# Kernel optimization log

Measured on AMD Instinct MI355X. Metric: run time of the kernel, lower is better.

## Reference

```python
import jax, jax.numpy as jnp
import numpy as np

B, T, S, I, H = 64, 64, 512, 512, 512

def setup_inputs() -> dict:
    key = jax.random.key(0)
    ks = jax.random.split(key, 9)
    sc = 0.02
    return {
        "input": jax.random.normal(ks[0], (B, T, I), jnp.float32),
        "h0": jax.random.normal(ks[1], (B, H), jnp.float32),
        "c0": jax.random.normal(ks[2], (B, H), jnp.float32),
        "ctx": jax.random.normal(ks[3], (S, B, H), jnp.float32),
        "W_ih": jax.random.normal(ks[4], (4 * H, I), jnp.float32) * sc,
        "b_ih": jax.random.normal(ks[5], (4 * H,), jnp.float32) * sc,
        "W_hh": jax.random.normal(ks[6], (4 * H, H), jnp.float32) * sc,
        "b_hh": jax.random.normal(ks[7], (4 * H,), jnp.float32) * sc,
        "W_out": jax.random.normal(ks[8], (H, 2 * H), jnp.float32) * sc,
    }

def reference(input, h0, c0, ctx, W_ih, b_ih, W_hh, b_hh, W_out):
    ctx_b = ctx.transpose(1, 0, 2)          # (B, S, H)
    x_tm = input.transpose(1, 0, 2)          # (T, B, I) time-major

    def step(carry, x):
        hx, cx = carry
        gates = x @ W_ih.T + b_ih + hx @ W_hh.T + b_hh   # (B, 4H)
        i, f, g, o = jnp.split(gates, 4, axis=1)          # chunk order: in, forget, cell, out
        ct = jax.nn.sigmoid(f) * cx + jax.nn.sigmoid(i) * jnp.tanh(g)
        ht = jax.nn.sigmoid(o) * jnp.tanh(ct)
        # dot attention over source positions
        scores = jnp.einsum('bsh,bh->bs', ctx_b, ht)      # (B, S)
        attn = jax.nn.softmax(scores, axis=1)
        wc = jnp.einsum('bs,bsh->bh', attn, ctx_b)        # (B, H)
        h_tilde = jnp.tanh(jnp.concatenate([wc, ht], axis=1) @ W_out.T)
        return (ht, ct), h_tilde

    (hT, cT), out = jax.lax.scan(step, (h0, c0), x_tm)    # out: (T, B, H)
    return out.transpose(1, 0, 2), hT, cT
```

## Files before the change

kernel.cpp:

```cpp
#include <hip/hip_runtime.h>
#include <hip/hip_bf16.h>

#define NB 64
#define NT_ 64
#define NS 512
#define NI 512
#define NH 512
#define G4 2048
#define H2 1024
#define BT (NB*NT_)
#define RBLK 64
#define CPB 8
#define XWB 512
#define TRB 4096
#define WOB 128
#define GRID_MEGA (RBLK + XWB + TRB + WOB)

typedef __attribute__((ext_vector_type(8))) short short8;
typedef __attribute__((ext_vector_type(4))) float f32x4;

__device__ __forceinline__ short f2bs(float f) {
    __hip_bfloat16 h = __float2bfloat16(f);
    return *reinterpret_cast<short*>(&h);
}
__device__ __forceinline__ float bs2f(short s) {
    unsigned int u = ((unsigned int)(unsigned short)s) << 16;
    union { unsigned int u; float f; } c; c.u = u; return c.f;
}
__device__ __forceinline__ short8 ld8b(const __hip_bfloat16* p) {
    return *reinterpret_cast<const short8*>(p);
}
__device__ __forceinline__ void ld8f2(const float* p, short8& hi, short8& lo) {
    float4 a = *reinterpret_cast<const float4*>(p);
    float4 b = *reinterpret_cast<const float4*>(p + 4);
    float v[8] = {a.x,a.y,a.z,a.w,b.x,b.y,b.z,b.w};
    #pragma unroll
    for (int i = 0; i < 8; i++) {
        short h = f2bs(v[i]);
        hi[i] = h;
        lo[i] = f2bs(v[i] - bs2f(h));
    }
}
__device__ __forceinline__ float fsigm(float x){ return 1.f/(1.f + __expf(-x)); }
__device__ __forceinline__ float ftanh(float x){ float e = __expf(2.f*x); return 1.f - 2.f/(e + 1.f); }

__global__ __launch_bounds__(256) void hseq0_init(const float* __restrict__ h0,
                                                  __hip_bfloat16* __restrict__ hs_h,
                                                  __hip_bfloat16* __restrict__ hs_l,
                                                  unsigned* __restrict__ sync) {
    int i = blockIdx.x*256 + threadIdx.x;
    if (i < 4096) sync[i] = 0u;
    if (i < NB*NH) {
        float x = h0[i];
        __hip_bfloat16 h = __float2bfloat16(x);
        hs_h[i] = h;
        hs_l[i] = __float2bfloat16(x - __bfloat162float(h));
    }
}

__global__ __launch_bounds__(256, 1) void lstm_mega(
    const float* __restrict__ c0,
    const float* __restrict__ W_hh,
    const float* __restrict__ input,
    const float* __restrict__ W_ih,
    const float* __restrict__ b_ih,
    const float* __restrict__ b_hh,
    float* __restrict__ XW2,
    __hip_bfloat16* __restrict__ hs_h,
    __hip_bfloat16* __restrict__ hs_l,
    float* __restrict__ hT, float* __restrict__ cT,
    unsigned* __restrict__ flags,
    unsigned* __restrict__ xwcnt,
    const float* __restrict__ ctx,
    __hip_bfloat16* __restrict__ ctxT,
    const float* __restrict__ W_out,
    __hip_bfloat16* __restrict__ Wout_h,
    __hip_bfloat16* __restrict__ Wout_l)
{
    __shared__ __align__(16) char smem_raw[82432];
    int bid = blockIdx.x;
    int tid = threadIdx.x;
    int lane = tid & 63, w = tid >> 6;
    int fr = lane & 15, fq = lane >> 4;

    if (bid < RBLK) {
        __hip_bfloat16* Wh = (__hip_bfloat16*)smem_raw;
        __hip_bfloat16* Wl = (__hip_bfloat16*)(smem_raw + 32768);
        float (*gl)[32][33] = (float(*)[32][33])(smem_raw + 65536);
        int bi = bid;
        {
            int jl = tid >> 3, ck8 = tid & 7;
            int grow = (jl >> 3) * NH + bi * CPB + (jl & 7);
            const float* src = W_hh + (size_t)grow * NH;
            #pragma unroll
            for (int cc = 0; cc < 8; cc++) {
                int ck = ck8 * 8 + cc;
                short8 hi, lo;
                ld8f2(src + ck*8, hi, lo);
                int sw = (ck * 16) ^ ((jl & 7) << 4);
                *(short8*)((char*)Wh + jl * 1024 + sw) = hi;
                *(short8*)((char*)Wl + jl * 1024 + sw) = lo;
            }
        }
        int eb  = tid >> 2;
        int ec0 = (tid & 3) * 2;
        int ebl = eb & 31, mhalf = eb >> 5;
        float creg[2];
        creg[0] = c0[eb * NH + bi*CPB + ec0];
        creg[1] = c0[eb * NH + bi*CPB + ec0 + 1];
        {
            int guard = 0;
            while (__hip_atomic_load(&xwcnt[0], __ATOMIC_RELAXED, __HIP_MEMORY_SCOPE_AGENT) < 8u) {
                __builtin_amdgcn_s_sleep(1);
                if (++guard > (1<<22)) break;
            }
        }
        float xw[8];
        #pragma unroll
        for (int g = 0; g < 4; g++)
          #pragma unroll
          for (int u = 0; u < 2; u++)
            xw[g*2+u] = XW2[(size_t)eb*G4 + g*NH + bi*CPB + ec0 + u];
        __syncthreads();

        int m0 = (w & 1) * 32;
        int kbase = (w >> 1) * 256;

        for (int t = 0; t < NT_; t++) {
            const __hip_bfloat16* Ah = hs_h + (size_t)t * NB * NH;
            const __hip_bfloat16* Al = hs_l + (size_t)t * NB * NH;
            short8 Aregh[2][8], Aregl[2][8];
            #pragma unroll
            for (int i = 0; i < 2; i++) {
                const __hip_bfloat16* rowH = Ah + (size_t)(m0 + i*16 + fr) * NH + kbase + fq*8;
                const __hip_bfloat16* rowL = Al + (size_t)(m0 + i*16 + fr) * NH + kbase + fq*8;
                #pragma unroll
                for (int k8 = 0; k8 < 8; k8++) {
                    Aregh[i][k8] = ld8b(rowH + k8*32);
                    Aregl[i][k8] = ld8b(rowL + k8*32);
                }
            }
            f32x4 acc[2][2] = {};
            #pragma unroll
            for (int k8 = 0; k8 < 8; k8++) {
                short8 b_h[2], b_l[2];
                #pragma unroll
                for (int j = 0; j < 2; j++) {
                    int jl = j*16 + fr;
                    int byt = jl*1024 + ((((kbase + k8*32 + fq*8)*2)) ^ ((jl & 7) << 4));
                    b_h[j] = *(const short8*)((const char*)Wh + byt);
                    b_l[j] = *(const short8*)((const char*)Wl + byt);
                }
                #pragma unroll
                for (int i = 0; i < 2; i++)
                    #pragma unroll
                    for (int j = 0; j < 2; j++) {
                        acc[i][j] = __builtin_amdgcn_mfma_f32_16x16x32_bf16(Aregh[i][k8], b_h[j], acc[i][j], 0,0,0);
                        acc[i][j] = __builtin_amdgcn_mfma_f32_16x16x32_bf16(Aregh[i][k8], b_l[j], acc[i][j], 0,0,0);
                        acc[i][j] = __builtin_amdgcn_mfma_f32_16x16x32_bf16(Aregl[i][k8], b_h[j], acc[i][j], 0,0,0);
                    }
            }
            #pragma unroll
            for (int i = 0; i < 2; i++)
              #pragma unroll
              for (int j = 0; j < 2; j++)
                #pragma unroll
                for (int r = 0; r < 4; r++)
                    gl[w][i*16 + fq*4 + r][j*16 + fr] = acc[i][j][r];
            __syncthreads();

            float hv[2];
            #pragma unroll
            for (int u = 0; u < 2; u++) {
                int cl = ec0 + u;
                float gi = gl[mhalf][ebl][cl]      + gl[2+mhalf][ebl][cl]      + xw[u];
                float gf = gl[mhalf][ebl][8 + cl]  + gl[2+mhalf][ebl][8 + cl]  + xw[2+u];
                float gg = gl[mhalf][ebl][16 + cl] + gl[2+mhalf][ebl][16 + cl] + xw[4+u];
                float go = gl[mhalf][ebl][24 + cl] + gl[2+mhalf][ebl][24 + cl] + xw[6+u];
                float ct = fsigm(gf)*creg[u] + fsigm(gi)*ftanh(gg);
                hv[u] = fsigm(go)*ftanh(ct);
                creg[u] = ct;
            }
            int hcol = bi*CPB + ec0;
            size_t hoff = (size_t)(t+1)*NB*NH + (size_t)eb*NH + hcol;
            unsigned short h0b = (unsigned short)f2bs(hv[0]);
            unsigned short h1b = (unsigned short)f2bs(hv[1]);
            unsigned ph = (unsigned)h0b | ((unsigned)h1b << 16);
            unsigned short l0b = (unsigned short)f2bs(hv[0] - bs2f((short)h0b));
            unsigned short l1b = (unsigned short)f2bs(hv[1] - bs2f((short)h1b));
            unsigned pl = (unsigned)l0b | ((unsigned)l1b << 16);
            __hip_atomic_store((unsigned*)&hs_h[hoff], ph, __ATOMIC_RELAXED, __HIP_MEMORY_SCOPE_AGENT);
            __hip_atomic_store((unsigned*)&hs_l[hoff], pl, __ATOMIC_RELAXED, __HIP_MEMORY_SCOPE_AGENT);
            if (t == NT_-1) {
                *(float2*)&hT[(size_t)eb*NH + hcol] = make_float2(hv[0], hv[1]);
                *(float2*)&cT[(size_t)eb*NH + hcol] = make_float2(creg[0], creg[1]);
            }
            asm volatile("s_waitcnt vmcnt(0)" ::: "memory");
            __syncthreads();
            if (tid == 0)
                __hip_atomic_store(&flags[bi*16], (unsigned)(t+1), __ATOMIC_RELAXED, __HIP_MEMORY_SCOPE_AGENT);
            if (t + 1 < NT_) {
                int guard = 0;
                while (__hip_atomic_load(&xwcnt[(t+1)*16], __ATOMIC_RELAXED, __HIP_MEMORY_SCOPE_AGENT) < 8u) {
                    __builtin_amdgcn_s_sleep(1);
                    if (++guard > (1<<22)) break;
                }
                #pragma unroll
                for (int g = 0; g < 4; g++)
                  #pragma unroll
                  for (int u = 0; u < 2; u++)
                    xw[g*2+u] = XW2[((size_t)(t+1)*NB + eb)*G4 + g*NH + bi*CPB + ec0 + u];
            }
            {
                unsigned target = (unsigned)(t+1);
                int guard = 0;
                while (__hip_atomic_load(&flags[lane*16], __ATOMIC_RELAXED, __HIP_MEMORY_SCOPE_AGENT) < target) {
                    __builtin_amdgcn_s_sleep(1);
                    if (++guard > (1<<22)) break;
                }
            }
        }
    } else if (bid < RBLK + XWB) {
        int e  = bid - RBLK;
        int t0 = e >> 3;
        int n0 = ((e & 7) * 4 + w) * 64;
        f32x4 acc[4][4] = {};
        for (int kk = 0; kk < NI; kk += 32) {
            short8 ah[4], al[4], bh[4], bl[4];
            #pragma unroll
            for (int i = 0; i < 4; i++)
                ld8f2(input + ((size_t)(i*16+fr)*NT_ + t0)*NI + kk + fq*8, ah[i], al[i]);
            #pragma unroll
            for (int j = 0; j < 4; j++)
                ld8f2(W_ih + (size_t)(n0+j*16+fr)*NI + kk + fq*8, bh[j], bl[j]);
            #pragma unroll
            for (int i = 0; i < 4; i++)
                #pragma unroll
                for (int j = 0; j < 4; j++) {
                    acc[i][j] = __builtin_amdgcn_mfma_f32_16x16x32_bf16(ah[i], bh[j], acc[i][j], 0,0,0);
                    acc[i][j] = __builtin_amdgcn_mfma_f32_16x16x32_bf16(ah[i], bl[j], acc[i][j], 0,0,0);
                    acc[i][j] = __builtin_amdgcn_mfma_f32_16x16x32_bf16(al[i], bh[j], acc[i][j], 0,0,0);
                }
        }
        #pragma unroll
        for (int i = 0; i < 4; i++)
          #pragma unroll
          for (int j = 0; j < 4; j++)
            #pragma unroll
            for (int r = 0; r < 4; r++) {
                int b = i*16 + fq*4 + r;
                int n = n0 + j*16 + fr;
                float v = acc[i][j][r] + b_ih[n] + b_hh[n];
                union { float f; unsigned u; } cv; cv.f = v;
                __hip_atomic_store((unsigned*)&XW2[((size_t)t0*NB + b)*G4 + n], cv.u,
                                   __ATOMIC_RELAXED, __HIP_MEMORY_SCOPE_AGENT);
            }
        asm volatile("s_waitcnt vmcnt(0)" ::: "memory");
        __syncthreads();
        if (tid == 0)
            __hip_atomic_fetch_add(&xwcnt[t0*16], 1u, __ATOMIC_RELAXED, __HIP_MEMORY_SCOPE_AGENT);
    } else if (bid < RBLK + XWB + TRB) {
        float (*tile)[65] = (float(*)[65])smem_raw;
        int tr = bid - (RBLK + XWB);
        int s0 = (tr & 7) * 64, h0 = ((tr >> 3) & 7) * 64, b = tr >> 6;
        int tx = tid & 63, ty = tid >> 6;
        for (int i = 0; i < 16; i++) {
            int s = i*4 + ty;
            tile[s][tx] = ctx[(size_t)(s0+s)*NB*NH + (size_t)b*NH + h0 + tx];
        }
        __syncthreads();
        for (int i = 0; i < 16; i++) {
            int h = i*4 + ty;
            ctxT[(size_t)b*NH*NS + (size_t)(h0+h)*NS + s0 + tx] = __float2bfloat16(tile[tx][h]);
        }
    } else {
        int wv = bid - (RBLK + XWB + TRB);
        for (int i = wv*256 + tid; i < NH*H2; i += WOB*256) {
            float x = W_out[i];
            __hip_bfloat16 h = __float2bfloat16(x);
            Wout_h[i] = h;
            Wout_l[i] = __float2bfloat16(x - __bfloat162float(h));
        }
    }
}

__global__ __launch_bounds__(256, 1) void attn_fused(
    const __hip_bfloat16* __restrict__ hs_h,
    const __hip_bfloat16* __restrict__ hs_l,
    const float* __restrict__ ctx,
    const __hip_bfloat16* __restrict__ ctxT,
    const __hip_bfloat16* __restrict__ Wout_h,
    const __hip_bfloat16* __restrict__ Wout_l,
    float* __restrict__ out)
{
    __shared__ __align__(16) char smem_raw[66560];
    float (*S)[520] = (float(*)[520])smem_raw;
    __hip_bfloat16 (*WcH)[520] = (__hip_bfloat16(*)[520])smem_raw;
    __hip_bfloat16 (*WcL)[520] = (__hip_bfloat16(*)[520])(smem_raw + 16640);
    __hip_bfloat16 (*AtH)[520] = (__hip_bfloat16(*)[520])(smem_raw + 33280);
    __hip_bfloat16 (*AtL)[520] = (__hip_bfloat16(*)[520])(smem_raw + 49920);

    int b  = blockIdx.x >> 2;
    int t0 = (blockIdx.x & 3) * 16;
    int tid = threadIdx.x;
    int lane = tid & 63, w = tid >> 6;
    int fr = lane & 15, fq = lane >> 4;

    {
        f32x4 sacc[8] = {};
        const __hip_bfloat16* Ab  = hs_h + (size_t)(t0+fr+1)*NB*NH + (size_t)b*NH;
        const __hip_bfloat16* Al2 = hs_l + (size_t)(t0+fr+1)*NB*NH + (size_t)b*NH;
        for (int kk = 0; kk < NH; kk += 32) {
            short8 ah = ld8b(Ab + kk + fq*8);
            short8 al = ld8b(Al2 + kk + fq*8);
            #pragma unroll
            for (int j = 0; j < 8; j++) {
                short8 bh, bl;
                ld8f2(ctx + (size_t)(w*128 + j*16 + fr)*NB*NH + (size_t)b*NH + kk + fq*8, bh, bl);
                sacc[j] = __builtin_amdgcn_mfma_f32_16x16x32_bf16(ah, bh, sacc[j], 0,0,0);
                sacc[j] = __builtin_amdgcn_mfma_f32_16x16x32_bf16(ah, bl, sacc[j], 0,0,0);
                sacc[j] = __builtin_amdgcn_mfma_f32_16x16x32_bf16(al, bh, sacc[j], 0,0,0);
            }
        }
        #pragma unroll
        for (int j = 0; j < 8; j++)
          #pragma unroll
          for (int r = 0; r < 4; r++)
            S[fq*4 + r][w*128 + j*16 + fr] = sacc[j][r];
    }
    __syncthreads();

    for (int rr = 0; rr < 4; rr++) {
        int row = w*4 + rr;
        float v[8], mx = -1e30f;
        #pragma unroll
        for (int i = 0; i < 8; i++) { v[i] = S[row][lane + i*64]; mx = fmaxf(mx, v[i]); }
        #pragma unroll
        for (int off = 32; off; off >>= 1) mx = fmaxf(mx, __shfl_xor(mx, off));
        float sum = 0.f;
        #pragma unroll
        for (int i = 0; i < 8; i++) { v[i] = __expf(v[i]-mx); sum += v[i]; }
        #pragma unroll
        for (int off = 32; off; off >>= 1) sum += __shfl_xor(sum, off);
        float inv = 1.f/sum;
        #pragma unroll
        for (int i = 0; i < 8; i++) {
            float a = v[i]*inv;
            short hb = f2bs(a);
            AtH[row][lane + i*64] = *(__hip_bfloat16*)&hb;
            short lb = f2bs(a - bs2f(hb));
            AtL[row][lane + i*64] = *(__hip_bfloat16*)&lb;
        }
    }
    __syncthreads();

    {
        f32x4 wacc[8] = {};
        const __hip_bfloat16* Bb = ctxT + (size_t)b*NH*NS;
        for (int kk = 0; kk < NS; kk += 32) {
            short8 pah = *(const short8*)&AtH[fr][kk + fq*8];
            short8 pal = *(const short8*)&AtL[fr][kk + fq*8];
            #pragma unroll
            for (int j = 0; j < 8; j++) {
                short8 cb = ld8b(Bb + (size_t)(w*128 + j*16 + fr)*NS + kk + fq*8);
                wacc[j] = __builtin_amdgcn_mfma_f32_16x16x32_bf16(pah, cb, wacc[j], 0,0,0);
                wacc[j] = __builtin_amdgcn_mfma_f32_16x16x32_bf16(pal, cb, wacc[j], 0,0,0);
            }
        }
        #pragma unroll
        for (int j = 0; j < 8; j++)
          #pragma unroll
          for (int r = 0; r < 4; r++) {
            float v = wacc[j][r];
            short hb = f2bs(v);
            WcH[fq*4 + r][w*128 + j*16 + fr] = *(__hip_bfloat16*)&hb;
            short lb = f2bs(v - bs2f(hb));
            WcL[fq*4 + r][w*128 + j*16 + fr] = *(__hip_bfloat16*)&lb;
          }
    }
    __syncthreads();

    {
        f32x4 oacc[8] = {};
        for (int kk = 0; kk < NH; kk += 32) {
            short8 ah = *(const short8*)&WcH[fr][kk + fq*8];
            short8 al = *(const short8*)&WcL[fr][kk + fq*8];
            #pragma unroll
            for (int j = 0; j < 8; j++) {
                size_t wrow = (size_t)(w*128 + j*16 + fr)*H2 + kk + fq*8;
                short8 bh = ld8b(Wout_h + wrow);
                short8 bl = ld8b(Wout_l + wrow);
                oacc[j] = __builtin_amdgcn_mfma_f32_16x16x32_bf16(ah, bh, oacc[j], 0,0,0);
                oacc[j] = __builtin_amdgcn_mfma_f32_16x16x32_bf16(ah, bl, oacc[j], 0,0,0);
                oacc[j] = __builtin_amdgcn_mfma_f32_16x16x32_bf16(al, bh, oacc[j], 0,0,0);
            }
        }
        const __hip_bfloat16* A2h = hs_h + (size_t)(t0+fr+1)*NB*NH + (size_t)b*NH;
        const __hip_bfloat16* A2l = hs_l + (size_t)(t0+fr+1)*NB*NH + (size_t)b*NH;
        for (int kk = 0; kk < NH; kk += 32) {
            short8 ah = ld8b(A2h + kk + fq*8);
            short8 al = ld8b(A2l + kk + fq*8);
            #pragma unroll
            for (int j = 0; j < 8; j++) {
                size_t wrow = (size_t)(w*128 + j*16 + fr)*H2 + NH + kk + fq*8;
                short8 bh = ld8b(Wout_h + wrow);
                short8 bl = ld8b(Wout_l + wrow);
                oacc[j] = __builtin_amdgcn_mfma_f32_16x16x32_bf16(ah, bh, oacc[j], 0,0,0);
                oacc[j] = __builtin_amdgcn_mfma_f32_16x16x32_bf16(ah, bl, oacc[j], 0,0,0);
                oacc[j] = __builtin_amdgcn_mfma_f32_16x16x32_bf16(al, bh, oacc[j], 0,0,0);
            }
        }
        #pragma unroll
        for (int j = 0; j < 8; j++)
          #pragma unroll
          for (int r = 0; r < 4; r++)
            out[(size_t)(b*64 + t0 + fq*4 + r)*NH + w*128 + j*16 + fr] = ftanh(oacc[j][r]);
    }
}


extern "C" void kernel_launch(void* const* d_in, const int* in_sizes, int n_in,
                              void* d_out, int out_size, void* d_ws, size_t ws_size,
                              hipStream_t stream) {
    const float* input = (const float*)d_in[0];
    const float* h0    = (const float*)d_in[1];
    const float* c0    = (const float*)d_in[2];
    const float* ctx   = (const float*)d_in[3];
    const float* W_ih  = (const float*)d_in[4];
    const float* b_ih  = (const float*)d_in[5];
    const float* W_hh  = (const float*)d_in[6];
    const float* b_hh  = (const float*)d_in[7];
    const float* W_out = (const float*)d_in[8];
    float* out = (float*)d_out;

    const size_t OFF_XW     = 0;
    const size_t OFF_HS_H   = 33554432;
    const size_t OFF_HS_L   = 37814272;
    const size_t OFF_SYNC   = 42074112;
    const size_t OFF_WOUT_H = 58859520;
    const size_t OFF_WOUT_L = 59908096;
    const size_t OFF_CTXT   = 60956672;
    if (ws_size < 94511104u) return;

    char* ws = (char*)d_ws;
    float*          XW2    = (float*)(ws + OFF_XW);
    __hip_bfloat16* hs_h   = (__hip_bfloat16*)(ws + OFF_HS_H);
    __hip_bfloat16* hs_l   = (__hip_bfloat16*)(ws + OFF_HS_L);
    unsigned*       sync   = (unsigned*)(ws + OFF_SYNC);
    unsigned*       flags  = sync;
    unsigned*       xwcnt  = sync + 1024;
    __hip_bfloat16* Wout_h = (__hip_bfloat16*)(ws + OFF_WOUT_H);
    __hip_bfloat16* Wout_l = (__hip_bfloat16*)(ws + OFF_WOUT_L);
    __hip_bfloat16* ctxT   = (__hip_bfloat16*)(ws + OFF_CTXT);

    hseq0_init<<<128, 256, 0, stream>>>(h0, hs_h, hs_l, sync);

    float* hT = out + (size_t)BT*NH;
    float* cT = hT + NB*NH;
    lstm_mega<<<GRID_MEGA, 256, 0, stream>>>(c0, W_hh, input, W_ih,
                                             b_ih, b_hh, XW2, hs_h, hs_l, hT, cT,
                                             flags, xwcnt, ctx, ctxT, W_out, Wout_h, Wout_l);

    attn_fused<<<256, 256, 0, stream>>>(hs_h, hs_l, ctx, ctxT, Wout_h, Wout_l, out);
}
```

Baseline: 614.9 us.

## Process 32 timesteps per block in attn_fused to double B-operand reuse

Each attention block now handles 32 query timesteps (two 16-row MFMA tiles) instead of 16, so every ctx, ctxT and W_out fragment loaded from global memory feeds twice as many MFMAs. This halves the grid to 128 blocks and doubles LDS use to about 130 KB, and an extra barrier guards the reuse of the score buffer. The cost is fewer blocks than CUs, so occupancy and parallelism drop, and register pressure from the doubled accumulators rises.

Result: no change. 621.8 us (+1.1%).

```diff
diff --git a/kernel.cpp b/kernel.cpp
--- a/kernel.cpp
+++ b/kernel.cpp
@@ -293,45 +293,59 @@
     const __hip_bfloat16* __restrict__ Wout_l,
     float* __restrict__ out)
 {
-    __shared__ __align__(16) char smem_raw[66560];
+    __shared__ __align__(16) char smem_raw[133120];
     float (*S)[520] = (float(*)[520])smem_raw;
     __hip_bfloat16 (*WcH)[520] = (__hip_bfloat16(*)[520])smem_raw;
-    __hip_bfloat16 (*WcL)[520] = (__hip_bfloat16(*)[520])(smem_raw + 16640);
-    __hip_bfloat16 (*AtH)[520] = (__hip_bfloat16(*)[520])(smem_raw + 33280);
-    __hip_bfloat16 (*AtL)[520] = (__hip_bfloat16(*)[520])(smem_raw + 49920);
-
-    int b  = blockIdx.x >> 2;
-    int t0 = (blockIdx.x & 3) * 16;
+    __hip_bfloat16 (*WcL)[520] = (__hip_bfloat16(*)[520])(smem_raw + 33280);
+    __hip_bfloat16 (*AtH)[520] = (__hip_bfloat16(*)[520])(smem_raw + 66560);
+    __hip_bfloat16 (*AtL)[520] = (__hip_bfloat16(*)[520])(smem_raw + 99840);
+
+    int b  = blockIdx.x >> 1;
+    int t0 = (blockIdx.x & 1) * 32;
     int tid = threadIdx.x;
     int lane = tid & 63, w = tid >> 6;
     int fr = lane & 15, fq = lane >> 4;
 
     {
-        f32x4 sacc[8] = {};
-        const __hip_bfloat16* Ab  = hs_h + (size_t)(t0+fr+1)*NB*NH + (size_t)b*NH;
-        const __hip_bfloat16* Al2 = hs_l + (size_t)(t0+fr+1)*NB*NH + (size_t)b*NH;
+        f32x4 sacc[2][8] = {};
+        const __hip_bfloat16* Abh[2];
+        const __hip_bfloat16* Abl[2];
+        #pragma unroll
+        for (int mi = 0; mi < 2; mi++) {
+            Abh[mi] = hs_h + (size_t)(t0 + mi*16 + fr + 1)*NB*NH + (size_t)b*NH;
+            Abl[mi] = hs_l + (size_t)(t0 + mi*16 + fr + 1)*NB*NH + (size_t)b*NH;
+        }
         for (int kk = 0; kk < NH; kk += 32) {
-            short8 ah = ld8b(Ab + kk + fq*8);
-            short8 al = ld8b(Al2 + kk + fq*8);
+            short8 ah[2], al[2];
+            #pragma unroll
+            for (int mi = 0; mi < 2; mi++) {
+                ah[mi] = ld8b(Abh[mi] + kk + fq*8);
+                al[mi] = ld8b(Abl[mi] + kk + fq*8);
+            }
             #pragma unroll
             for (int j = 0; j < 8; j++) {
                 short8 bh, bl;
                 ld8f2(ctx + (size_t)(w*128 + j*16 + fr)*NB*NH + (size_t)b*NH + kk + fq*8, bh, bl);
-                sacc[j] = __builtin_amdgcn_mfma_f32_16x16x32_bf16(ah, bh, sacc[j], 0,0,0);
-                sacc[j] = __builtin_amdgcn_mfma_f32_16x16x32_bf16(ah, bl, sacc[j], 0,0,0);
-                sacc[j] = __builtin_amdgcn_mfma_f32_16x16x32_bf16(al, bh, sacc[j], 0,0,0);
-            }
-        }
-        #pragma unroll
-        for (int j = 0; j < 8; j++)
+                #pragma unroll
+                for (int mi = 0; mi < 2; mi++) {
+                    sacc[mi][j] = __builtin_amdgcn_mfma_f32_16x16x32_bf16(ah[mi], bh, sacc[mi][j], 0,0,0);
+                    sacc[mi][j] = __builtin_amdgcn_mfma_f32_16x16x32_bf16(ah[mi], bl, sacc[mi][j], 0,0,0);
+                    sacc[mi][j] = __builtin_amdgcn_mfma_f32_16x16x32_bf16(al[mi], bh, sacc[mi][j], 0,0,0);
+                }
+            }
+        }
+        #pragma unroll
+        for (int mi = 0; mi < 2; mi++)
           #pragma unroll
-          for (int r = 0; r < 4; r++)
-            S[fq*4 + r][w*128 + j*16 + fr] = sacc[j][r];
+          for (int j = 0; j < 8; j++)
+            #pragma unroll
+            for (int r = 0; r < 4; r++)
+                S[mi*16 + fq*4 + r][w*128 + j*16 + fr] = sacc[mi][j][r];
     }
     __syncthreads();
 
-    for (int rr = 0; rr < 4; rr++) {
-        int row = w*4 + rr;
+    for (int rr = 0; rr < 8; rr++) {
+        int row = w*8 + rr;
         float v[8], mx = -1e30f;
         #pragma unroll
         for (int i = 0; i < 8; i++) { v[i] = S[row][lane + i*64]; mx = fmaxf(mx, v[i]); }
@@ -355,66 +369,90 @@
     __syncthreads();
 
     {
-        f32x4 wacc[8] = {};
+        f32x4 wacc[2][8] = {};
         const __hip_bfloat16* Bb = ctxT + (size_t)b*NH*NS;
         for (int kk = 0; kk < NS; kk += 32) {
-            short8 pah = *(const short8*)&AtH[fr][kk + fq*8];
-            short8 pal = *(const short8*)&AtL[fr][kk + fq*8];
+            short8 pah[2], pal[2];
+            #pragma unroll
+            for (int mi = 0; mi < 2; mi++) {
+                pah[mi] = *(const short8*)&AtH[mi*16 + fr][kk + fq*8];
+                pal[mi] = *(const short8*)&AtL[mi*16 + fr][kk + fq*8];
+            }
             #pragma unroll
             for (int j = 0; j < 8; j++) {
                 short8 cb = ld8b(Bb + (size_t)(w*128 + j*16 + fr)*NS + kk + fq*8);
-                wacc[j] = __builtin_amdgcn_mfma_f32_16x16x32_bf16(pah, cb, wacc[j], 0,0,0);
-                wacc[j] = __builtin_amdgcn_mfma_f32_16x16x32_bf16(pal, cb, wacc[j], 0,0,0);
-            }
-        }
-        #pragma unroll
-        for (int j = 0; j < 8; j++)
+                #pragma unroll
+                for (int mi = 0; mi < 2; mi++) {
+                    wacc[mi][j] = __builtin_amdgcn_mfma_f32_16x16x32_bf16(pah[mi], cb, wacc[mi][j], 0,0,0);
+                    wacc[mi][j] = __builtin_amdgcn_mfma_f32_16x16x32_bf16(pal[mi], cb, wacc[mi][j], 0,0,0);
+                }
+            }
+        }
+        __syncthreads();
+        #pragma unroll
+        for (int mi = 0; mi < 2; mi++)
           #pragma unroll
-          for (int r = 0; r < 4; r++) {
-            float v = wacc[j][r];
-            short hb = f2bs(v);
-            WcH[fq*4 + r][w*128 + j*16 + fr] = *(__hip_bfloat16*)&hb;
-            short lb = f2bs(v - bs2f(hb));
-            WcL[fq*4 + r][w*128 + j*16 + fr] = *(__hip_bfloat16*)&lb;
-          }
+          for (int j = 0; j < 8; j++)
+            #pragma unroll
+            for (int r = 0; r < 4; r++) {
+                float v = wacc[mi][j][r];
+                short hb = f2bs(v);
+                WcH[mi*16 + fq*4 + r][w*128 + j*16 + fr] = *(__hip_bfloat16*)&hb;
+                short lb = f2bs(v - bs2f(hb));
+                WcL[mi*16 + fq*4 + r][w*128 + j*16 + fr] = *(__hip_bfloat16*)&lb;
+            }
     }
     __syncthreads();
 
     {
-        f32x4 oacc[8] = {};
+        f32x4 oacc[2][8] = {};
         for (int kk = 0; kk < NH; kk += 32) {
-            short8 ah = *(const short8*)&WcH[fr][kk + fq*8];
-            short8 al = *(const short8*)&WcL[fr][kk + fq*8];
+            short8 ah[2], al[2];
+            #pragma unroll
+            for (int mi = 0; mi < 2; mi++) {
+                ah[mi] = *(const short8*)&WcH[mi*16 + fr][kk + fq*8];
+                al[mi] = *(const short8*)&WcL[mi*16 + fr][kk + fq*8];
+            }
             #pragma unroll
             for (int j = 0; j < 8; j++) {
                 size_t wrow = (size_t)(w*128 + j*16 + fr)*H2 + kk + fq*8;
                 short8 bh = ld8b(Wout_h + wrow);
                 short8 bl = ld8b(Wout_l + wrow);
-                oacc[j] = __builtin_amdgcn_mfma_f32_16x16x32_bf16(ah, bh, oacc[j], 0,0,0);
-                oacc[j] = __builtin_amdgcn_mfma_f32_16x16x32_bf16(ah, bl, oacc[j], 0,0,0);
-                oacc[j] = __builtin_amdgcn_mfma_f32_16x16x32_bf16(al, bh, oacc[j], 0,0,0);
-            }
-        }
-        const __hip_bfloat16* A2h = hs_h + (size_t)(t0+fr+1)*NB*NH + (size_t)b*NH;
-        const __hip_bfloat16* A2l = hs_l + (size_t)(t0+fr+1)*NB*NH + (size_t)b*NH;
+                #pragma unroll
+                for (int mi = 0; mi < 2; mi++) {
+                    oacc[mi][j] = __builtin_amdgcn_mfma_f32_16x16x32_bf16(ah[mi], bh, oacc[mi][j], 0,0,0);
+                    oacc[mi][j] = __builtin_amdgcn_mfma_f32_16x16x32_bf16(ah[mi], bl, oacc[mi][j], 0,0,0);
+                    oacc[mi][j] = __builtin_amdgcn_mfma_f32_16x16x32_bf16(al[mi], bh, oacc[mi][j], 0,0,0);
+                }
+            }
+        }
         for (int kk = 0; kk < NH; kk += 32) {
-            short8 ah = ld8b(A2h + kk + fq*8);
-            short8 al = ld8b(A2l + kk + fq*8);
+            short8 ah[2], al[2];
+            #pragma unroll
+            for (int mi = 0; mi < 2; mi++) {
+                ah[mi] = ld8b(hs_h + (size_t)(t0 + mi*16 + fr + 1)*NB*NH + (size_t)b*NH + kk + fq*8);
+                al[mi] = ld8b(hs_l + (size_t)(t0 + mi*16 + fr + 1)*NB*NH + (size_t)b*NH + kk + fq*8);
+            }
             #pragma unroll
             for (int j = 0; j < 8; j++) {
                 size_t wrow = (size_t)(w*128 + j*16 + fr)*H2 + NH + kk + fq*8;
                 short8 bh = ld8b(Wout_h + wrow);
                 short8 bl = ld8b(Wout_l + wrow);
-                oacc[j] = __builtin_amdgcn_mfma_f32_16x16x32_bf16(ah, bh, oacc[j], 0,0,0);
-                oacc[j] = __builtin_amdgcn_mfma_f32_16x16x32_bf16(ah, bl, oacc[j], 0,0,0);
-                oacc[j] = __builtin_amdgcn_mfma_f32_16x16x32_bf16(al, bh, oacc[j], 0,0,0);
-            }
-        }
-        #pragma unroll
-        for (int j = 0; j < 8; j++)
+                #pragma unroll
+                for (int mi = 0; mi < 2; mi++) {
+                    oacc[mi][j] = __builtin_amdgcn_mfma_f32_16x16x32_bf16(ah[mi], bh, oacc[mi][j], 0,0,0);
+                    oacc[mi][j] = __builtin_amdgcn_mfma_f32_16x16x32_bf16(ah[mi], bl, oacc[mi][j], 0,0,0);
+                    oacc[mi][j] = __builtin_amdgcn_mfma_f32_16x16x32_bf16(al[mi], bh, oacc[mi][j], 0,0,0);
+                }
+            }
+        }
+        #pragma unroll
+        for (int mi = 0; mi < 2; mi++)
           #pragma unroll
-          for (int r = 0; r < 4; r++)
-            out[(size_t)(b*64 + t0 + fq*4 + r)*NH + w*128 + j*16 + fr] = ftanh(oacc[j][r]);
+          for (int j = 0; j < 8; j++)
+            #pragma unroll
+            for (int r = 0; r < 4; r++)
+                out[(size_t)(b*64 + t0 + mi*16 + fq*4 + r)*NH + w*128 + j*16 + fr] = ftanh(oacc[mi][j][r]);
     }
 }
 
@@ -461,5 +499,5 @@
                                              b_ih, b_hh, XW2, hs_h, hs_l, hT, cT,
                                              flags, xwcnt, ctx, ctxT, W_out, Wout_h, Wout_l);
 
-    attn_fused<<<256, 256, 0, stream>>>(hs_h, hs_l, ctx, ctxT, Wout_h, Wout_l, out);
-}
+    attn_fused<<<128, 256, 0, stream>>>(hs_h, hs_l, ctx, ctxT, Wout_h, Wout_l, out);
+}
```
